# Kernel tuning notes

Hardware: AMD Instinct MI355X
Metric: run time of the kernel (lower is better)

The kernel has to match this reference:

```python
import jax, jax.numpy as jnp
import numpy as np

B, N, F, D, H, T = 32, 1024, 32, 64, 64, 4


def setup_inputs() -> dict:
    key = jax.random.key(0)
    ks = jax.random.split(key, 12)
    def w(k, shape):
        return 0.01 * jax.random.normal(k, shape, dtype=jnp.float32)
    z = lambda *s: jnp.zeros(s, jnp.float32)
    return {
        "xv": jax.random.normal(ks[0], (B, N, F), dtype=jnp.float32),
        "option": jax.random.uniform(ks[1], (B, 1), dtype=jnp.float32),
        "adj": jax.random.normal(ks[2], (N, N), dtype=jnp.float32),
        "mu1": w(ks[3], (F, D)),
        "W2": w(ks[4], (D, D)), "b2": z(D),
        "W3": w(ks[5], (D, D)), "b3": z(D),
        "W4": w(ks[6], (D, 1)), "b4": z(D),
        "Wq1": w(ks[7], (D, D)), "bq1": z(D),
        "Wq2": w(ks[8], (D, 1)), "bq2": z(D),
        "Wreg": w(ks[9], (H, 2 * D)), "breg": z(H),
        "Wq": w(ks[10], (1, H)), "bq": z(1),
    }


def reference(xv, option, adj, mu1, W2, b2, W3, b3, W4, b4,
              Wq1, bq1, Wq2, bq2, Wreg, breg, Wq, bq):
    # binary adjacency for message passing, raw weights for the mu_4 branch
    A = (adj > 0).astype(xv.dtype)                       # [N,N]
    mu_1 = jnp.maximum(xv @ mu1, 0.0)                    # [B,N,D]
    # mu_4: Linear(1,D) over every edge weight, clamp, sum over neighbors
    # (identical value every round t>=1, so computed once)
    mu4 = jnp.maximum(adj[..., None] * W4[:, 0] + b4, 0.0).sum(axis=1)[None]  # [1,N,D]
    mu3 = mu4 @ W3.T + b3                                # [1,N,D]
    mu = mu_1                                            # t = 0
    for _ in range(1, T):                                # t = 1..T-1
        mu_pool = jnp.einsum('nm,bmd->bnd', A, mu)       # neighbor aggregation
        mu2 = mu_pool @ W2.T + b2
        mu = jnp.maximum(mu_1 + mu2 + mu3, 0.0)
    mu_mean = jnp.maximum(mu.mean(axis=1, keepdims=True) @ Wq1.T + bq1, 0.0)  # [B,1,D]
    mu_aug = jnp.concatenate([mu, mu_mean], axis=1)      # [B,N+1,D]
    q2 = option.reshape(B, 1, 1) @ Wq2.T + bq2           # [B,1,D]
    q2 = jnp.broadcast_to(q2, (B, N + 1, D))
    q_ = jnp.concatenate([mu_aug, q2], axis=-1)          # [B,N+1,2D]
    qreg = jnp.maximum(q_ @ Wreg.T + breg, 0.0)          # [B,N+1,H]
    return qreg @ Wq.T + bq                              # [B,N+1,1]
```

## Files before the change

kernel.cpp:

```cpp
#include <hip/hip_runtime.h>
#include <hip/hip_bf16.h>

#define Bc 32
#define Nc 1024
#define Fc 32
#define Dc 64
#define Hc 64

typedef __bf16 bf16;
typedef __bf16 bf16x4 __attribute__((ext_vector_type(4)));
typedef __bf16 bf16x8 __attribute__((ext_vector_type(8)));
typedef float  f32x4  __attribute__((ext_vector_type(4)));

#define AS_STRIDE 136
#define MS_STRIDE 72
#define LDS_MAIN  (2 * 64 * AS_STRIDE * 2)
#define LDS_NONF  (LDS_MAIN + 2 * 64 * MS_STRIDE * 2)
#define LDS_FIN   (LDS_NONF + 2 * 64 * MS_STRIDE * 2)

__global__ void k_prep(const float* __restrict__ adj, const float* __restrict__ W2,
                       const float* __restrict__ option, const float* __restrict__ Wq2,
                       const float* __restrict__ bq2, const float* __restrict__ Wreg,
                       const float* __restrict__ breg,
                       bf16* __restrict__ Abf, bf16* __restrict__ W2bf,
                       float* __restrict__ c2base, float* __restrict__ musum) {
    const int t = threadIdx.x;
    if (blockIdx.x < 1024) {
        const int i = blockIdx.x * 1024 + t * 4;
        const float4 a = *(const float4*)&adj[i];
        bf16x4 o;
        o[0] = (bf16)((a.x > 0.f) ? 1.f : 0.f);
        o[1] = (bf16)((a.y > 0.f) ? 1.f : 0.f);
        o[2] = (bf16)((a.z > 0.f) ? 1.f : 0.f);
        o[3] = (bf16)((a.w > 0.f) ? 1.f : 0.f);
        *(bf16x4*)&Abf[i] = o;
    } else if (blockIdx.x == 1024) {
        for (int j = t * 16; j < t * 16 + 16; ++j) W2bf[j] = (bf16)W2[j];
    } else {
        for (int i = t; i < 2048; i += 256) musum[i] = 0.f;
        for (int i = t; i < 2048; i += 256) {
            const int b = i >> 6, h = i & 63;
            const float opt = option[b];
            float a = breg[h];
#pragma unroll
            for (int j = 0; j < 64; ++j)
                a = fmaf(fmaf(opt, Wq2[j], bq2[j]), Wreg[h * 128 + 64 + j], a);
            c2base[i] = a;
        }
    }
}

__global__ void k_c3(const float* __restrict__ adj, const float* __restrict__ W4,
                     const float* __restrict__ b4, const float* __restrict__ W3,
                     const float* __restrict__ b3, const float* __restrict__ b2,
                     float* __restrict__ C3) {
    const int n = blockIdx.x, t = threadIdx.x;
    const int e = t & 63, g = t >> 6;
    __shared__ float red[256];
    __shared__ float mu4_s[64];
    const float w4e = W4[e], b4e = b4[e];
    const float* arow = adj + (size_t)n * Nc;
    float acc = 0.f;
    for (int m = g * 256; m < g * 256 + 256; ++m)
        acc += fmaxf(fmaf(arow[m], w4e, b4e), 0.f);
    red[t] = acc;
    __syncthreads();
    if (g == 0) mu4_s[e] = red[e] + red[64 + e] + red[128 + e] + red[192 + e];
    __syncthreads();
    if (t < 64) {
        const int d = t;
        float a = b3[d] + b2[d];
        for (int ee = 0; ee < 64; ++ee) a = fmaf(mu4_s[ee], W3[d * 64 + ee], a);
        C3[n * 64 + d] = a;
    }
}

__global__ void k_mu1(const float* __restrict__ xv, const float* __restrict__ w,
                      const bf16* __restrict__ W2bf,
                      float* __restrict__ mu_1, bf16* __restrict__ Xt) {
    const int nb = blockIdx.x, b = blockIdx.y, t = threadIdx.x;
    const int n0 = nb * 64;
    __shared__ float w_s[Fc * Dc];
    __shared__ float x_s[64 * 33];
    __shared__ bf16  muS[64 * MS_STRIDE];
    __shared__ bf16  W2s[64 * MS_STRIDE];
    for (int i = t; i < Fc * Dc; i += 256) w_s[i] = w[i];
    for (int i = t; i < 64 * Fc; i += 256) {
        int r = i >> 5, f = i & 31;
        x_s[r * 33 + f] = xv[((size_t)b * Nc + n0 + r) * Fc + f];
    }
#pragma unroll
    for (int i = 0; i < 2; ++i) {
        int g = i * 256 + t, row = g >> 3, c = g & 7;
        *(bf16x8*)&W2s[row * MS_STRIDE + c * 8] = *(const bf16x8*)&W2bf[row * 64 + c * 8];
    }
    __syncthreads();
    const int d = t & 63, rg = t >> 6;
    for (int ri = 0; ri < 16; ++ri) {
        int r = rg * 16 + ri;
        float acc = 0.f;
#pragma unroll
        for (int f = 0; f < Fc; ++f) acc = fmaf(x_s[r * 33 + f], w_s[f * Dc + d], acc);
        acc = fmaxf(acc, 0.f);
        mu_1[((size_t)b * Nc + n0 + r) * Dc + d] = acc;
        muS[r * MS_STRIDE + d] = (bf16)acc;
    }
    __syncthreads();
    const int l = t & 63, wv = t >> 6, lm = l & 15, q = l >> 4;
    f32x4 xacc[4];
#pragma unroll
    for (int ct = 0; ct < 4; ++ct)
#pragma unroll
        for (int r = 0; r < 4; ++r) xacc[ct][r] = 0.f;
#pragma unroll
    for (int s = 0; s < 2; ++s) {
        bf16x8 a = *(const bf16x8*)&muS[(wv * 16 + lm) * MS_STRIDE + s * 32 + q * 8];
#pragma unroll
        for (int ct = 0; ct < 4; ++ct) {
            bf16x8 bv = *(const bf16x8*)&W2s[(ct * 16 + lm) * MS_STRIDE + s * 32 + q * 8];
            xacc[ct] = __builtin_amdgcn_mfma_f32_16x16x32_bf16(a, bv, xacc[ct], 0, 0, 0);
        }
    }
#pragma unroll
    for (int ct = 0; ct < 4; ++ct) {
        const int dd = ct * 16 + lm;
        bf16x4 p;
#pragma unroll
        for (int r = 0; r < 4; ++r) p[r] = (bf16)xacc[ct][r];
        *(bf16x4*)&Xt[(size_t)b * 65536 + (size_t)dd * 1024 + n0 + wv * 16 + q * 4] = p;
    }
}

template <bool FINAL>
__global__ __launch_bounds__(256, 2)
void k_round(const bf16* __restrict__ Abf, const bf16* __restrict__ Xt_in,
             const float* __restrict__ mu_1, const float* __restrict__ C3,
             const bf16* __restrict__ W2bf, bf16* __restrict__ Xt_out,
             const float* __restrict__ Wreg, const float* __restrict__ c2base,
             const float* __restrict__ Wq, const float* __restrict__ bq,
             float* __restrict__ musum, float* __restrict__ out) {
    const int b = blockIdx.x, nb = blockIdx.y, t = threadIdx.x;
    const int n0 = nb * 64;
    const int l = t & 63, wv = t >> 6, lm = l & 15, q = l >> 4;
    extern __shared__ char smem[];
    bf16* As   = (bf16*)smem;
    bf16* Xs   = As + 64 * AS_STRIDE;
    bf16* muHi = Xs + 64 * AS_STRIDE;
    bf16* WHi  = muHi + 64 * MS_STRIDE;
    bf16* muLo = WHi + 64 * MS_STRIDE;
    bf16* WLo  = muLo + 64 * MS_STRIDE;

    if (!FINAL) {
#pragma unroll
        for (int i = 0; i < 2; ++i) {
            int g = i * 256 + t, row = g >> 3, c = g & 7;
            *(bf16x8*)&WHi[row * MS_STRIDE + c * 8] = *(const bf16x8*)&W2bf[row * 64 + c * 8];
        }
    } else {
#pragma unroll
        for (int i = 0; i < 4; ++i) {
            int g = i * 1024 + t * 4;
            int h = g >> 6, d = g & 63;
            const float4 w4 = *(const float4*)&Wreg[h * 128 + d];
            bf16x4 ohi, olo;
            ohi[0] = (bf16)w4.x; olo[0] = (bf16)(w4.x - (float)ohi[0]);
            ohi[1] = (bf16)w4.y; olo[1] = (bf16)(w4.y - (float)ohi[1]);
            ohi[2] = (bf16)w4.z; olo[2] = (bf16)(w4.z - (float)ohi[2]);
            ohi[3] = (bf16)w4.w; olo[3] = (bf16)(w4.w - (float)ohi[3]);
            *(bf16x4*)&WHi[h * MS_STRIDE + d] = ohi;
            *(bf16x4*)&WLo[h * MS_STRIDE + d] = olo;
        }
    }

    f32x4 acc[4];
#pragma unroll
    for (int ct = 0; ct < 4; ++ct)
#pragma unroll
        for (int r = 0; r < 4; ++r) acc[ct][r] = 0.f;

    const bf16* Arow = Abf + (size_t)n0 * 1024;
    const bf16* Xrow = Xt_in + (size_t)b * 65536;

    bf16x8 pa[4], px[4];
#pragma unroll
    for (int i = 0; i < 4; ++i) {
        int g = i * 256 + t, row = g >> 4, c = g & 15;
        pa[i] = *(const bf16x8*)&Arow[(size_t)row * 1024 + c * 8];
        px[i] = *(const bf16x8*)&Xrow[(size_t)row * 1024 + c * 8];
    }

    for (int kc = 0; kc < 1024; kc += 128) {
        __syncthreads();
#pragma unroll
        for (int i = 0; i < 4; ++i) {
            int g = i * 256 + t, row = g >> 4, c = g & 15;
            *(bf16x8*)&As[row * AS_STRIDE + c * 8] = pa[i];
            *(bf16x8*)&Xs[row * AS_STRIDE + c * 8] = px[i];
        }
        __syncthreads();
        if (kc + 128 < 1024) {
#pragma unroll
            for (int i = 0; i < 4; ++i) {
                int g = i * 256 + t, row = g >> 4, c = g & 15;
                pa[i] = *(const bf16x8*)&Arow[(size_t)row * 1024 + kc + 128 + c * 8];
                px[i] = *(const bf16x8*)&Xrow[(size_t)row * 1024 + kc + 128 + c * 8];
            }
        }
#pragma unroll
        for (int s = 0; s < 4; ++s) {
            bf16x8 a = *(const bf16x8*)&As[(wv * 16 + lm) * AS_STRIDE + s * 32 + q * 8];
#pragma unroll
            for (int ct = 0; ct < 4; ++ct) {
                bf16x8 bv = *(const bf16x8*)&Xs[(ct * 16 + lm) * AS_STRIDE + s * 32 + q * 8];
                acc[ct] = __builtin_amdgcn_mfma_f32_16x16x32_bf16(a, bv, acc[ct], 0, 0, 0);
            }
        }
    }

    float vals[4][4];
#pragma unroll
    for (int ct = 0; ct < 4; ++ct) {
        const int col = ct * 16 + lm;
#pragma unroll
        for (int r = 0; r < 4; ++r) {
            const int n = n0 + wv * 16 + q * 4 + r;
            float v = mu_1[((size_t)b * Nc + n) * Dc + col] + acc[ct][r] + C3[n * 64 + col];
            vals[ct][r] = fmaxf(v, 0.f);
        }
    }

    __syncthreads();
#pragma unroll
    for (int ct = 0; ct < 4; ++ct) {
        const int col = ct * 16 + lm;
#pragma unroll
        for (int r = 0; r < 4; ++r) {
            const int row = wv * 16 + q * 4 + r;
            const float v = vals[ct][r];
            const bf16 hi = (bf16)v;
            muHi[row * MS_STRIDE + col] = hi;
            if (FINAL) muLo[row * MS_STRIDE + col] = (bf16)(v - (float)hi);
        }
    }

    if (FINAL) {
#pragma unroll
        for (int ct = 0; ct < 4; ++ct) {
            float s = vals[ct][0] + vals[ct][1] + vals[ct][2] + vals[ct][3];
            s += __shfl_xor(s, 16);
            s += __shfl_xor(s, 32);
            if (q == 0) atomicAdd(&musum[b * 64 + ct * 16 + lm], s);
        }
    }

    __syncthreads();
    f32x4 xacc[4];
#pragma unroll
    for (int ct = 0; ct < 4; ++ct)
#pragma unroll
        for (int r = 0; r < 4; ++r) xacc[ct][r] = 0.f;

    if (!FINAL) {
#pragma unroll
        for (int s = 0; s < 2; ++s) {
            bf16x8 a = *(const bf16x8*)&muHi[(wv * 16 + lm) * MS_STRIDE + s * 32 + q * 8];
#pragma unroll
            for (int ct = 0; ct < 4; ++ct) {
                bf16x8 bv = *(const bf16x8*)&WHi[(ct * 16 + lm) * MS_STRIDE + s * 32 + q * 8];
                xacc[ct] = __builtin_amdgcn_mfma_f32_16x16x32_bf16(a, bv, xacc[ct], 0, 0, 0);
            }
        }
#pragma unroll
        for (int ct = 0; ct < 4; ++ct) {
            const int dd = ct * 16 + lm;
            bf16x4 p;
#pragma unroll
            for (int r = 0; r < 4; ++r) p[r] = (bf16)xacc[ct][r];
            *(bf16x4*)&Xt_out[(size_t)b * 65536 + (size_t)dd * 1024 + n0 + wv * 16 + q * 4] = p;
        }
    } else {
#pragma unroll
        for (int s = 0; s < 2; ++s) {
            const int aoff = (wv * 16 + lm) * MS_STRIDE + s * 32 + q * 8;
            bf16x8 aHi = *(const bf16x8*)&muHi[aoff];
            bf16x8 aLo = *(const bf16x8*)&muLo[aoff];
#pragma unroll
            for (int ct = 0; ct < 4; ++ct) {
                const int boff = (ct * 16 + lm) * MS_STRIDE + s * 32 + q * 8;
                bf16x8 bHi = *(const bf16x8*)&WHi[boff];
                bf16x8 bLo = *(const bf16x8*)&WLo[boff];
                xacc[ct] = __builtin_amdgcn_mfma_f32_16x16x32_bf16(aHi, bHi, xacc[ct], 0, 0, 0);
                xacc[ct] = __builtin_amdgcn_mfma_f32_16x16x32_bf16(aLo, bHi, xacc[ct], 0, 0, 0);
                xacc[ct] = __builtin_amdgcn_mfma_f32_16x16x32_bf16(aHi, bLo, xacc[ct], 0, 0, 0);
            }
        }
        const float bq0 = bq[0];
        float rowsum[4] = {0.f, 0.f, 0.f, 0.f};
#pragma unroll
        for (int ct = 0; ct < 4; ++ct) {
            const int h = ct * 16 + lm;
            const float c2 = c2base[b * 64 + h];
            const float wqh = Wq[h];
#pragma unroll
            for (int r = 0; r < 4; ++r)
                rowsum[r] += fmaxf(xacc[ct][r] + c2, 0.f) * wqh;
        }
#pragma unroll
        for (int r = 0; r < 4; ++r) {
            float v = rowsum[r];
            v += __shfl_xor(v, 1);
            v += __shfl_xor(v, 2);
            v += __shfl_xor(v, 4);
            v += __shfl_xor(v, 8);
            if (lm == 0) {
                const int n = n0 + wv * 16 + q * 4 + r;
                out[(size_t)b * (Nc + 1) + n] = v + bq0;
            }
        }
    }
}

__global__ void k_tail(const float* __restrict__ musum, const float* __restrict__ Wq1,
                       const float* __restrict__ bq1, const float* __restrict__ Wreg,
                       const float* __restrict__ c2base, const float* __restrict__ Wq,
                       const float* __restrict__ bq, float* __restrict__ out) {
    const int b = blockIdx.x, l = threadIdx.x;
    __shared__ float mean_s[64];
    __shared__ float mp[64];
    mean_s[l] = musum[b * 64 + l] * (1.f / Nc);
    __syncthreads();
    float a = bq1[l];
#pragma unroll
    for (int e = 0; e < 64; ++e) a = fmaf(mean_s[e], Wq1[l * 64 + e], a);
    mp[l] = fmaxf(a, 0.f);
    __syncthreads();
    float h = c2base[b * 64 + l];
#pragma unroll
    for (int d = 0; d < 64; ++d) h = fmaf(mp[d], Wreg[l * 128 + d], h);
    float v = fmaxf(h, 0.f) * Wq[l];
#pragma unroll
    for (int off = 32; off; off >>= 1) v += __shfl_down(v, off);
    if (l == 0) out[(size_t)b * (Nc + 1) + Nc] = v + bq[0];
}

extern "C" void kernel_launch(void* const* d_in, const int* in_sizes, int n_in,
                              void* d_out, int out_size, void* d_ws, size_t ws_size,
                              hipStream_t stream) {
    const float* xv     = (const float*)d_in[0];
    const float* option = (const float*)d_in[1];
    const float* adj    = (const float*)d_in[2];
    const float* mu1w   = (const float*)d_in[3];
    const float* W2     = (const float*)d_in[4];
    const float* b2     = (const float*)d_in[5];
    const float* W3     = (const float*)d_in[6];
    const float* b3     = (const float*)d_in[7];
    const float* W4     = (const float*)d_in[8];
    const float* b4     = (const float*)d_in[9];
    const float* Wq1    = (const float*)d_in[10];
    const float* bq1    = (const float*)d_in[11];
    const float* Wq2    = (const float*)d_in[12];
    const float* bq2    = (const float*)d_in[13];
    const float* Wreg   = (const float*)d_in[14];
    const float* breg   = (const float*)d_in[15];
    const float* Wq     = (const float*)d_in[16];
    const float* bq     = (const float*)d_in[17];
    float* out = (float*)d_out;

    float* ws = (float*)d_ws;
    const size_t MU = (size_t)Bc * Nc * Dc;
    float* mu_1     = ws;
    float* C3       = ws + MU;
    float* c2base   = C3 + 65536;
    float* musum    = c2base + 2048;
    bf16*  Abf      = (bf16*)(musum + 2048);
    bf16*  W2bf     = Abf + (size_t)Nc * Nc;
    bf16*  Xt0      = W2bf + 4096;
    bf16*  Xt1      = Xt0 + MU;

    k_prep<<<1026, 256, 0, stream>>>(adj, W2, option, Wq2, bq2, Wreg, breg,
                                     Abf, W2bf, c2base, musum);
    k_c3<<<Nc, 256, 0, stream>>>(adj, W4, b4, W3, b3, b2, C3);
    k_mu1<<<dim3(Nc / 64, Bc), 256, 0, stream>>>(xv, mu1w, W2bf, mu_1, Xt0);
    k_round<false><<<dim3(Bc, Nc / 64), 256, LDS_NONF, stream>>>(
        Abf, Xt0, mu_1, C3, W2bf, Xt1,
        nullptr, nullptr, nullptr, nullptr, nullptr, nullptr);
    k_round<false><<<dim3(Bc, Nc / 64), 256, LDS_NONF, stream>>>(
        Abf, Xt1, mu_1, C3, W2bf, Xt0,
        nullptr, nullptr, nullptr, nullptr, nullptr, nullptr);
    k_round<true><<<dim3(Bc, Nc / 64), 256, LDS_FIN, stream>>>(
        Abf, Xt0, mu_1, C3, nullptr, nullptr,
        Wreg, c2base, Wq, bq, musum, out);
    k_tail<<<Bc, 64, 0, stream>>>(musum, Wq1, bq1, Wreg, c2base, Wq, bq, out);
}
```

Baseline: 175.1 us.

## Fuse prep kernels, MFMA mu1, halve round tile rows with LDS aliasing

Merges the adjacency binarization and the C3 (mu4/W3) computation into one kernel, so adj is read once and one launch is dropped. The mu1 projection moves from scalar FMA to split bf16 hi/lo MFMA. The round kernels switch to 32-row tiles with a 2x2 wave split, alias the epilogue LDS buffers over the main-loop buffers to cut LDS use, and raise launch bounds to 4 blocks per CU for occupancy. The trade-off is that A tiles are now shared across half as many rows, so X tiles are reloaded twice as often, and the final kernel needs an extra LDS reduction and barrier.

```diff
diff --git a/kernel.cpp b/kernel.cpp
--- a/kernel.cpp
+++ b/kernel.cpp
@@ -14,29 +14,59 @@
 
 #define AS_STRIDE 136
 #define MS_STRIDE 72
-#define LDS_MAIN  (2 * 64 * AS_STRIDE * 2)
-#define LDS_NONF  (LDS_MAIN + 2 * 64 * MS_STRIDE * 2)
-#define LDS_FIN   (LDS_NONF + 2 * 64 * MS_STRIDE * 2)
-
-__global__ void k_prep(const float* __restrict__ adj, const float* __restrict__ W2,
-                       const float* __restrict__ option, const float* __restrict__ Wq2,
-                       const float* __restrict__ bq2, const float* __restrict__ Wreg,
-                       const float* __restrict__ breg,
-                       bf16* __restrict__ Abf, bf16* __restrict__ W2bf,
-                       float* __restrict__ c2base, float* __restrict__ musum) {
+
+#define LDS_RND_NONF 26112
+#define LDS_RND_FIN  27904
+
+__global__ void k_pc(const float* __restrict__ adj, const float* __restrict__ W4,
+                     const float* __restrict__ b4, const float* __restrict__ W3,
+                     const float* __restrict__ b3, const float* __restrict__ b2,
+                     const float* __restrict__ W2, const float* __restrict__ option,
+                     const float* __restrict__ Wq2, const float* __restrict__ bq2,
+                     const float* __restrict__ Wreg, const float* __restrict__ breg,
+                     bf16* __restrict__ Abf, float* __restrict__ C3,
+                     bf16* __restrict__ W2bf, float* __restrict__ c2base,
+                     float* __restrict__ musum) {
     const int t = threadIdx.x;
     if (blockIdx.x < 1024) {
-        const int i = blockIdx.x * 1024 + t * 4;
-        const float4 a = *(const float4*)&adj[i];
-        bf16x4 o;
-        o[0] = (bf16)((a.x > 0.f) ? 1.f : 0.f);
-        o[1] = (bf16)((a.y > 0.f) ? 1.f : 0.f);
-        o[2] = (bf16)((a.z > 0.f) ? 1.f : 0.f);
-        o[3] = (bf16)((a.w > 0.f) ? 1.f : 0.f);
-        *(bf16x4*)&Abf[i] = o;
-    } else if (blockIdx.x == 1024) {
+        const int n = blockIdx.x;
+        const float* arow = adj + (size_t)n * Nc;
+        {
+            const float4 a = *(const float4*)&arow[t * 4];
+            bf16x4 o;
+            o[0] = (bf16)((a.x > 0.f) ? 1.f : 0.f);
+            o[1] = (bf16)((a.y > 0.f) ? 1.f : 0.f);
+            o[2] = (bf16)((a.z > 0.f) ? 1.f : 0.f);
+            o[3] = (bf16)((a.w > 0.f) ? 1.f : 0.f);
+            *(bf16x4*)&Abf[(size_t)n * Nc + t * 4] = o;
+        }
+        const int e = t & 63, g = t >> 6;
+        __shared__ float red[256];
+        __shared__ float mu4_s[64];
+        const float w4e = W4[e], b4e = b4[e];
+        float acc = 0.f;
+        const float4* arow4 = (const float4*)(arow + g * 256);
+#pragma unroll 8
+        for (int j = 0; j < 64; ++j) {
+            const float4 av = arow4[j];
+            acc += fmaxf(fmaf(av.x, w4e, b4e), 0.f);
+            acc += fmaxf(fmaf(av.y, w4e, b4e), 0.f);
+            acc += fmaxf(fmaf(av.z, w4e, b4e), 0.f);
+            acc += fmaxf(fmaf(av.w, w4e, b4e), 0.f);
+        }
+        red[t] = acc;
+        __syncthreads();
+        if (g == 0) mu4_s[e] = red[e] + red[64 + e] + red[128 + e] + red[192 + e];
+        __syncthreads();
+        if (t < 64) {
+            const int d = t;
+            float a = b3[d] + b2[d];
+#pragma unroll
+            for (int ee = 0; ee < 64; ++ee) a = fmaf(mu4_s[ee], W3[d * 64 + ee], a);
+            C3[n * 64 + d] = a;
+        }
+    } else {
         for (int j = t * 16; j < t * 16 + 16; ++j) W2bf[j] = (bf16)W2[j];
-    } else {
         for (int i = t; i < 2048; i += 256) musum[i] = 0.f;
         for (int i = t; i < 2048; i += 256) {
             const int b = i >> 6, h = i & 63;
@@ -50,44 +80,38 @@
     }
 }
 
-__global__ void k_c3(const float* __restrict__ adj, const float* __restrict__ W4,
-                     const float* __restrict__ b4, const float* __restrict__ W3,
-                     const float* __restrict__ b3, const float* __restrict__ b2,
-                     float* __restrict__ C3) {
-    const int n = blockIdx.x, t = threadIdx.x;
-    const int e = t & 63, g = t >> 6;
-    __shared__ float red[256];
-    __shared__ float mu4_s[64];
-    const float w4e = W4[e], b4e = b4[e];
-    const float* arow = adj + (size_t)n * Nc;
-    float acc = 0.f;
-    for (int m = g * 256; m < g * 256 + 256; ++m)
-        acc += fmaxf(fmaf(arow[m], w4e, b4e), 0.f);
-    red[t] = acc;
-    __syncthreads();
-    if (g == 0) mu4_s[e] = red[e] + red[64 + e] + red[128 + e] + red[192 + e];
-    __syncthreads();
-    if (t < 64) {
-        const int d = t;
-        float a = b3[d] + b2[d];
-        for (int ee = 0; ee < 64; ++ee) a = fmaf(mu4_s[ee], W3[d * 64 + ee], a);
-        C3[n * 64 + d] = a;
-    }
-}
-
 __global__ void k_mu1(const float* __restrict__ xv, const float* __restrict__ w,
                       const bf16* __restrict__ W2bf,
                       float* __restrict__ mu_1, bf16* __restrict__ Xt) {
     const int nb = blockIdx.x, b = blockIdx.y, t = threadIdx.x;
     const int n0 = nb * 64;
-    __shared__ float w_s[Fc * Dc];
-    __shared__ float x_s[64 * 33];
-    __shared__ bf16  muS[64 * MS_STRIDE];
-    __shared__ bf16  W2s[64 * MS_STRIDE];
-    for (int i = t; i < Fc * Dc; i += 256) w_s[i] = w[i];
-    for (int i = t; i < 64 * Fc; i += 256) {
-        int r = i >> 5, f = i & 31;
-        x_s[r * 33 + f] = xv[((size_t)b * Nc + n0 + r) * Fc + f];
+    const int l = t & 63, wv = t >> 6, lm = l & 15, q = l >> 4;
+    __shared__ bf16 xhi[64 * 40], xlo[64 * 40];
+    __shared__ bf16 whi[64 * 40], wlo[64 * 40];
+    __shared__ bf16 muS[64 * MS_STRIDE];
+    __shared__ bf16 W2s[64 * MS_STRIDE];
+
+    {
+        const int row = t >> 2, f0 = (t & 3) * 8;
+        const float* src = &xv[((size_t)b * Nc + n0 + row) * Fc + f0];
+        const float4 v0 = *(const float4*)src;
+        const float4 v1 = *(const float4*)(src + 4);
+        bf16x8 hi, lo;
+        float vv[8] = {v0.x, v0.y, v0.z, v0.w, v1.x, v1.y, v1.z, v1.w};
+#pragma unroll
+        for (int j = 0; j < 8; ++j) { hi[j] = (bf16)vv[j]; lo[j] = (bf16)(vv[j] - (float)hi[j]); }
+        *(bf16x8*)&xhi[row * 40 + f0] = hi;
+        *(bf16x8*)&xlo[row * 40 + f0] = lo;
+    }
+    {
+        const int d = t >> 2, f0 = (t & 3) * 8;
+#pragma unroll
+        for (int j = 0; j < 8; ++j) {
+            const float v = w[(f0 + j) * Dc + d];
+            const bf16 hi = (bf16)v;
+            whi[d * 40 + f0 + j] = hi;
+            wlo[d * 40 + f0 + j] = (bf16)(v - (float)hi);
+        }
     }
 #pragma unroll
     for (int i = 0; i < 2; ++i) {
@@ -95,18 +119,36 @@
         *(bf16x8*)&W2s[row * MS_STRIDE + c * 8] = *(const bf16x8*)&W2bf[row * 64 + c * 8];
     }
     __syncthreads();
-    const int d = t & 63, rg = t >> 6;
-    for (int ri = 0; ri < 16; ++ri) {
-        int r = rg * 16 + ri;
-        float acc = 0.f;
-#pragma unroll
-        for (int f = 0; f < Fc; ++f) acc = fmaf(x_s[r * 33 + f], w_s[f * Dc + d], acc);
-        acc = fmaxf(acc, 0.f);
-        mu_1[((size_t)b * Nc + n0 + r) * Dc + d] = acc;
-        muS[r * MS_STRIDE + d] = (bf16)acc;
-    }
-    __syncthreads();
-    const int l = t & 63, wv = t >> 6, lm = l & 15, q = l >> 4;
+
+    f32x4 acc[4];
+#pragma unroll
+    for (int ct = 0; ct < 4; ++ct)
+#pragma unroll
+        for (int r = 0; r < 4; ++r) acc[ct][r] = 0.f;
+    {
+        const bf16x8 aHi = *(const bf16x8*)&xhi[(wv * 16 + lm) * 40 + q * 8];
+        const bf16x8 aLo = *(const bf16x8*)&xlo[(wv * 16 + lm) * 40 + q * 8];
+#pragma unroll
+        for (int ct = 0; ct < 4; ++ct) {
+            const bf16x8 bHi = *(const bf16x8*)&whi[(ct * 16 + lm) * 40 + q * 8];
+            const bf16x8 bLo = *(const bf16x8*)&wlo[(ct * 16 + lm) * 40 + q * 8];
+            acc[ct] = __builtin_amdgcn_mfma_f32_16x16x32_bf16(aHi, bHi, acc[ct], 0, 0, 0);
+            acc[ct] = __builtin_amdgcn_mfma_f32_16x16x32_bf16(aLo, bHi, acc[ct], 0, 0, 0);
+            acc[ct] = __builtin_amdgcn_mfma_f32_16x16x32_bf16(aHi, bLo, acc[ct], 0, 0, 0);
+        }
+    }
+#pragma unroll
+    for (int ct = 0; ct < 4; ++ct) {
+        const int col = ct * 16 + lm;
+#pragma unroll
+        for (int r = 0; r < 4; ++r) {
+            const int row = wv * 16 + q * 4 + r;
+            const float v = fmaxf(acc[ct][r], 0.f);
+            mu_1[((size_t)b * Nc + n0 + row) * Dc + col] = v;
+            muS[row * MS_STRIDE + col] = (bf16)v;
+        }
+    }
+    __syncthreads();
     f32x4 xacc[4];
 #pragma unroll
     for (int ct = 0; ct < 4; ++ct)
@@ -132,7 +174,7 @@
 }
 
 template <bool FINAL>
-__global__ __launch_bounds__(256, 2)
+__global__ __launch_bounds__(256, 4)
 void k_round(const bf16* __restrict__ Abf, const bf16* __restrict__ Xt_in,
              const float* __restrict__ mu_1, const float* __restrict__ C3,
              const bf16* __restrict__ W2bf, bf16* __restrict__ Xt_out,
@@ -140,21 +182,25 @@
              const float* __restrict__ Wq, const float* __restrict__ bq,
              float* __restrict__ musum, float* __restrict__ out) {
     const int b = blockIdx.x, nb = blockIdx.y, t = threadIdx.x;
-    const int n0 = nb * 64;
+    const int n0 = nb * 32;
     const int l = t & 63, wv = t >> 6, lm = l & 15, q = l >> 4;
+    const int rw = wv & 1, cth = wv >> 1;
     extern __shared__ char smem[];
     bf16* As   = (bf16*)smem;
-    bf16* Xs   = As + 64 * AS_STRIDE;
-    bf16* muHi = Xs + 64 * AS_STRIDE;
-    bf16* WHi  = muHi + 64 * MS_STRIDE;
-    bf16* muLo = WHi + 64 * MS_STRIDE;
-    bf16* WLo  = muLo + 64 * MS_STRIDE;
-
+    bf16* Xs   = (bf16*)(smem + 8704);
+    bf16* muHi = (bf16*)smem;
+    bf16* WHi  = (bf16*)(smem + 4608);
+    bf16* muLo = (bf16*)(smem + 13824);
+    bf16* WLo  = (bf16*)(smem + 18432);
+    float* rpart = (float*)(smem + 27648);
+
+    bf16x8 pw[2];
+    bf16x4 wrhi[4], wrlo[4];
     if (!FINAL) {
 #pragma unroll
         for (int i = 0; i < 2; ++i) {
             int g = i * 256 + t, row = g >> 3, c = g & 7;
-            *(bf16x8*)&WHi[row * MS_STRIDE + c * 8] = *(const bf16x8*)&W2bf[row * 64 + c * 8];
+            pw[i] = *(const bf16x8*)&W2bf[row * 64 + c * 8];
         }
     } else {
 #pragma unroll
@@ -162,131 +208,154 @@
             int g = i * 1024 + t * 4;
             int h = g >> 6, d = g & 63;
             const float4 w4 = *(const float4*)&Wreg[h * 128 + d];
-            bf16x4 ohi, olo;
-            ohi[0] = (bf16)w4.x; olo[0] = (bf16)(w4.x - (float)ohi[0]);
-            ohi[1] = (bf16)w4.y; olo[1] = (bf16)(w4.y - (float)ohi[1]);
-            ohi[2] = (bf16)w4.z; olo[2] = (bf16)(w4.z - (float)ohi[2]);
-            ohi[3] = (bf16)w4.w; olo[3] = (bf16)(w4.w - (float)ohi[3]);
-            *(bf16x4*)&WHi[h * MS_STRIDE + d] = ohi;
-            *(bf16x4*)&WLo[h * MS_STRIDE + d] = olo;
-        }
-    }
-
-    f32x4 acc[4];
-#pragma unroll
-    for (int ct = 0; ct < 4; ++ct)
+            wrhi[i][0] = (bf16)w4.x; wrlo[i][0] = (bf16)(w4.x - (float)wrhi[i][0]);
+            wrhi[i][1] = (bf16)w4.y; wrlo[i][1] = (bf16)(w4.y - (float)wrhi[i][1]);
+            wrhi[i][2] = (bf16)w4.z; wrlo[i][2] = (bf16)(w4.z - (float)wrhi[i][2]);
+            wrhi[i][3] = (bf16)w4.w; wrlo[i][3] = (bf16)(w4.w - (float)wrhi[i][3]);
+        }
+    }
+
+    f32x4 acc[2];
+#pragma unroll
+    for (int ct = 0; ct < 2; ++ct)
 #pragma unroll
         for (int r = 0; r < 4; ++r) acc[ct][r] = 0.f;
 
     const bf16* Arow = Abf + (size_t)n0 * 1024;
     const bf16* Xrow = Xt_in + (size_t)b * 65536;
 
-    bf16x8 pa[4], px[4];
+    bf16x8 pa[2], px[4];
+#pragma unroll
+    for (int i = 0; i < 2; ++i) {
+        int g = i * 256 + t, row = g >> 4, c = g & 15;
+        pa[i] = *(const bf16x8*)&Arow[(size_t)row * 1024 + c * 8];
+    }
 #pragma unroll
     for (int i = 0; i < 4; ++i) {
         int g = i * 256 + t, row = g >> 4, c = g & 15;
-        pa[i] = *(const bf16x8*)&Arow[(size_t)row * 1024 + c * 8];
         px[i] = *(const bf16x8*)&Xrow[(size_t)row * 1024 + c * 8];
     }
 
     for (int kc = 0; kc < 1024; kc += 128) {
         __syncthreads();
 #pragma unroll
+        for (int i = 0; i < 2; ++i) {
+            int g = i * 256 + t, row = g >> 4, c = g & 15;
+            *(bf16x8*)&As[row * AS_STRIDE + c * 8] = pa[i];
+        }
+#pragma unroll
         for (int i = 0; i < 4; ++i) {
             int g = i * 256 + t, row = g >> 4, c = g & 15;
-            *(bf16x8*)&As[row * AS_STRIDE + c * 8] = pa[i];
             *(bf16x8*)&Xs[row * AS_STRIDE + c * 8] = px[i];
         }
         __syncthreads();
         if (kc + 128 < 1024) {
 #pragma unroll
+            for (int i = 0; i < 2; ++i) {
+                int g = i * 256 + t, row = g >> 4, c = g & 15;
+                pa[i] = *(const bf16x8*)&Arow[(size_t)row * 1024 + kc + 128 + c * 8];
+            }
+#pragma unroll
             for (int i = 0; i < 4; ++i) {
                 int g = i * 256 + t, row = g >> 4, c = g & 15;
-                pa[i] = *(const bf16x8*)&Arow[(size_t)row * 1024 + kc + 128 + c * 8];
                 px[i] = *(const bf16x8*)&Xrow[(size_t)row * 1024 + kc + 128 + c * 8];
             }
         }
 #pragma unroll
         for (int s = 0; s < 4; ++s) {
-            bf16x8 a = *(const bf16x8*)&As[(wv * 16 + lm) * AS_STRIDE + s * 32 + q * 8];
-#pragma unroll
-            for (int ct = 0; ct < 4; ++ct) {
-                bf16x8 bv = *(const bf16x8*)&Xs[(ct * 16 + lm) * AS_STRIDE + s * 32 + q * 8];
+            bf16x8 a = *(const bf16x8*)&As[(rw * 16 + lm) * AS_STRIDE + s * 32 + q * 8];
+#pragma unroll
+            for (int ct = 0; ct < 2; ++ct) {
+                bf16x8 bv = *(const bf16x8*)&Xs[(cth * 32 + ct * 16 + lm) * AS_STRIDE + s * 32 + q * 8];
                 acc[ct] = __builtin_amdgcn_mfma_f32_16x16x32_bf16(a, bv, acc[ct], 0, 0, 0);
             }
         }
     }
 
-    float vals[4][4];
-#pragma unroll
-    for (int ct = 0; ct < 4; ++ct) {
-        const int col = ct * 16 + lm;
+    float vals[2][4];
+#pragma unroll
+    for (int ct = 0; ct < 2; ++ct) {
+        const int col = cth * 32 + ct * 16 + lm;
 #pragma unroll
         for (int r = 0; r < 4; ++r) {
-            const int n = n0 + wv * 16 + q * 4 + r;
+            const int n = n0 + rw * 16 + q * 4 + r;
             float v = mu_1[((size_t)b * Nc + n) * Dc + col] + acc[ct][r] + C3[n * 64 + col];
             vals[ct][r] = fmaxf(v, 0.f);
         }
     }
 
     __syncthreads();
-#pragma unroll
-    for (int ct = 0; ct < 4; ++ct) {
-        const int col = ct * 16 + lm;
+    if (!FINAL) {
+#pragma unroll
+        for (int i = 0; i < 2; ++i) {
+            int g = i * 256 + t, row = g >> 3, c = g & 7;
+            *(bf16x8*)&WHi[row * MS_STRIDE + c * 8] = pw[i];
+        }
+    } else {
+#pragma unroll
+        for (int i = 0; i < 4; ++i) {
+            int g = i * 1024 + t * 4;
+            int h = g >> 6, d = g & 63;
+            *(bf16x4*)&WHi[h * MS_STRIDE + d] = wrhi[i];
+            *(bf16x4*)&WLo[h * MS_STRIDE + d] = wrlo[i];
+        }
+    }
+#pragma unroll
+    for (int ct = 0; ct < 2; ++ct) {
+        const int col = cth * 32 + ct * 16 + lm;
 #pragma unroll
         for (int r = 0; r < 4; ++r) {
-            const int row = wv * 16 + q * 4 + r;
+            const int row = rw * 16 + q * 4 + r;
             const float v = vals[ct][r];
             const bf16 hi = (bf16)v;
             muHi[row * MS_STRIDE + col] = hi;
             if (FINAL) muLo[row * MS_STRIDE + col] = (bf16)(v - (float)hi);
         }
     }
-
     if (FINAL) {
 #pragma unroll
-        for (int ct = 0; ct < 4; ++ct) {
+        for (int ct = 0; ct < 2; ++ct) {
             float s = vals[ct][0] + vals[ct][1] + vals[ct][2] + vals[ct][3];
             s += __shfl_xor(s, 16);
             s += __shfl_xor(s, 32);
-            if (q == 0) atomicAdd(&musum[b * 64 + ct * 16 + lm], s);
-        }
-    }
-
-    __syncthreads();
-    f32x4 xacc[4];
-#pragma unroll
-    for (int ct = 0; ct < 4; ++ct)
+            if (q == 0) atomicAdd(&musum[b * 64 + cth * 32 + ct * 16 + lm], s);
+        }
+    }
+    __syncthreads();
+
+    f32x4 xacc[2];
+#pragma unroll
+    for (int ct = 0; ct < 2; ++ct)
 #pragma unroll
         for (int r = 0; r < 4; ++r) xacc[ct][r] = 0.f;
 
     if (!FINAL) {
 #pragma unroll
         for (int s = 0; s < 2; ++s) {
-            bf16x8 a = *(const bf16x8*)&muHi[(wv * 16 + lm) * MS_STRIDE + s * 32 + q * 8];
-#pragma unroll
-            for (int ct = 0; ct < 4; ++ct) {
-                bf16x8 bv = *(const bf16x8*)&WHi[(ct * 16 + lm) * MS_STRIDE + s * 32 + q * 8];
+            bf16x8 a = *(const bf16x8*)&muHi[(rw * 16 + lm) * MS_STRIDE + s * 32 + q * 8];
+#pragma unroll
+            for (int ct = 0; ct < 2; ++ct) {
+                bf16x8 bv = *(const bf16x8*)&WHi[(cth * 32 + ct * 16 + lm) * MS_STRIDE + s * 32 + q * 8];
                 xacc[ct] = __builtin_amdgcn_mfma_f32_16x16x32_bf16(a, bv, xacc[ct], 0, 0, 0);
             }
         }
 #pragma unroll
-        for (int ct = 0; ct < 4; ++ct) {
-            const int dd = ct * 16 + lm;
+        for (int ct = 0; ct < 2; ++ct) {
+            const int dd = cth * 32 + ct * 16 + lm;
             bf16x4 p;
 #pragma unroll
             for (int r = 0; r < 4; ++r) p[r] = (bf16)xacc[ct][r];
-            *(bf16x4*)&Xt_out[(size_t)b * 65536 + (size_t)dd * 1024 + n0 + wv * 16 + q * 4] = p;
+            *(bf16x4*)&Xt_out[(size_t)b * 65536 + (size_t)dd * 1024 + n0 + rw * 16 + q * 4] = p;
         }
     } else {
 #pragma unroll
         for (int s = 0; s < 2; ++s) {
-            const int aoff = (wv * 16 + lm) * MS_STRIDE + s * 32 + q * 8;
+            const int aoff = (rw * 16 + lm) * MS_STRIDE + s * 32 + q * 8;
             bf16x8 aHi = *(const bf16x8*)&muHi[aoff];
             bf16x8 aLo = *(const bf16x8*)&muLo[aoff];
 #pragma unroll
-            for (int ct = 0; ct < 4; ++ct) {
-                const int boff = (ct * 16 + lm) * MS_STRIDE + s * 32 + q * 8;
+            for (int ct = 0; ct < 2; ++ct) {
+                const int boff = (cth * 32 + ct * 16 + lm) * MS_STRIDE + s * 32 + q * 8;
                 bf16x8 bHi = *(const bf16x8*)&WHi[boff];
                 bf16x8 bLo = *(const bf16x8*)&WLo[boff];
                 xacc[ct] = __builtin_amdgcn_mfma_f32_16x16x32_bf16(aHi, bHi, xacc[ct], 0, 0, 0);
@@ -294,11 +363,10 @@
                 xacc[ct] = __builtin_amdgcn_mfma_f32_16x16x32_bf16(aHi, bLo, xacc[ct], 0, 0, 0);
             }
         }
-        const float bq0 = bq[0];
         float rowsum[4] = {0.f, 0.f, 0.f, 0.f};
 #pragma unroll
-        for (int ct = 0; ct < 4; ++ct) {
-            const int h = ct * 16 + lm;
+        for (int ct = 0; ct < 2; ++ct) {
+            const int h = cth * 32 + ct * 16 + lm;
             const float c2 = c2base[b * 64 + h];
             const float wqh = Wq[h];
 #pragma unroll
@@ -312,11 +380,11 @@
             v += __shfl_xor(v, 2);
             v += __shfl_xor(v, 4);
             v += __shfl_xor(v, 8);
-            if (lm == 0) {
-                const int n = n0 + wv * 16 + q * 4 + r;
-                out[(size_t)b * (Nc + 1) + n] = v + bq0;
-            }
-        }
+            if (lm == 0) rpart[cth * 32 + rw * 16 + q * 4 + r] = v;
+        }
+        __syncthreads();
+        if (t < 32)
+            out[(size_t)b * (Nc + 1) + n0 + t] = rpart[t] + rpart[32 + t] + bq[0];
     }
 }
 
@@ -377,17 +445,16 @@
     bf16*  Xt0      = W2bf + 4096;
     bf16*  Xt1      = Xt0 + MU;
 
-    k_prep<<<1026, 256, 0, stream>>>(adj, W2, option, Wq2, bq2, Wreg, breg,
-                                     Abf, W2bf, c2base, musum);
-    k_c3<<<Nc, 256, 0, stream>>>(adj, W4, b4, W3, b3, b2, C3);
+    k_pc<<<1025, 256, 0, stream>>>(adj, W4, b4, W3, b3, b2, W2, option, Wq2, bq2,
+                                   Wreg, breg, Abf, C3, W2bf, c2base, musum);
     k_mu1<<<dim3(Nc / 64, Bc), 256, 0, stream>>>(xv, mu1w, W2bf, mu_1, Xt0);
-    k_round<false><<<dim3(Bc, Nc / 64), 256, LDS_NONF, stream>>>(
+    k_round<false><<<dim3(Bc, Nc / 32), 256, LDS_RND_NONF, stream>>>(
         Abf, Xt0, mu_1, C3, W2bf, Xt1,
         nullptr, nullptr, nullptr, nullptr, nullptr, nullptr);
-    k_round<false><<<dim3(Bc, Nc / 64), 256, LDS_NONF, stream>>>(
+    k_round<false><<<dim3(Bc, Nc / 32), 256, LDS_RND_NONF, stream>>>(
         Abf, Xt1, mu_1, C3, W2bf, Xt0,
         nullptr, nullptr, nullptr, nullptr, nullptr, nullptr);
-    k_round<true><<<dim3(Bc, Nc / 64), 256, LDS_FIN, stream>>>(
+    k_round<true><<<dim3(Bc, Nc / 32), 256, LDS_RND_FIN, stream>>>(
         Abf, Xt0, mu_1, C3, nullptr, nullptr,
         Wreg, c2base, Wq, bq, musum, out);
     k_tail<<<Bc, 64, 0, stream>>>(musum, Wq1, bq1, Wreg, c2base, Wq, bq, out);
```

Result: faster. 159.3 us (-9.0%).
